# Kernel optimization log

Measured on AMD Instinct MI355X. Metric: run time of the kernel, lower is better.

Reference implementation:

```python
import math
import jax, jax.numpy as jnp
import numpy as np

B, N, D = 8, 2048, 512


def setup_inputs() -> dict:
    key = jax.random.key(0)
    ks = jax.random.split(key, 9)
    s = 1.0 / math.sqrt(D)
    return {
        "x": jax.random.normal(ks[0], (B, N, D), dtype=jnp.float32),
        "adj": jax.random.uniform(ks[1], (B, N, N), dtype=jnp.float32),
        "Wqk": jax.random.normal(ks[2], (D, D), dtype=jnp.float32) * s,
        "bqk": jax.random.normal(ks[3], (D,), dtype=jnp.float32) * s,
        "Wl": jax.random.normal(ks[4], (D, D), dtype=jnp.float32) * s,
        "bl": jax.random.normal(ks[5], (D,), dtype=jnp.float32) * s,
        "Wr": jax.random.normal(ks[6], (D, D), dtype=jnp.float32) * s,
        "Wd": jax.random.normal(ks[7], (D, 1), dtype=jnp.float32),
        "bd": jax.random.normal(ks[8], (D,), dtype=jnp.float32),
    }


def reference(x, adj, Wqk, bqk, Wl, bl, Wr, Wd, bd):
    # degree gating: sigmoid(Linear(rowsum(adj)))
    deg = jnp.sum(adj, axis=-1, keepdims=True)           # [B, N, 1]
    gate = jax.nn.sigmoid(deg * Wd[:, 0] + bd)           # [B, N, D]
    xg = x * gate
    # sigmoid QK features
    QK = jax.nn.sigmoid(xg @ Wqk.T + bqk)                # [B, N, D]
    scores = jnp.einsum("bnd,bmd->bnm", QK, QK) / math.sqrt(D)
    scores = scores * adj                                # adjacency mask
    attn = scores / (jnp.sum(scores, axis=-1, keepdims=True) + 1e-6)
    out = jnp.einsum("bnm,bmd->bnd", attn, xg)           # aggregate values
    out = out @ Wl.T + bl + xg @ Wr.T                    # left + right branch
    return jax.nn.relu(out)
```

## Files before the change

### kernel.cpp

```cpp
#include <hip/hip_runtime.h>
#include <hip/hip_bf16.h>


typedef __bf16 bf16;
typedef __bf16 bf16x8 __attribute__((ext_vector_type(8)));
typedef float  f32x4  __attribute__((ext_vector_type(4)));

#define Bb 8
#define Nn 2048
#define Dd 512
#define SMEM_BYTES 33792

__device__ __forceinline__ bf16 to_bf16(float f) { return (bf16)f; }
__device__ __forceinline__ float sigmoidf_(float x) { return 1.0f / (1.0f + __expf(-x)); }

__device__ __forceinline__ void gld16(const void* g, void* l) {
    __builtin_amdgcn_global_load_lds(
        (__attribute__((address_space(1))) void*)(void*)g,
        (__attribute__((address_space(3))) void*)l,
        16, 0, 0);
}

__device__ __forceinline__ void gemm_bt_core(
    const bf16* __restrict__ A, const bf16* __restrict__ Bt,
    int lda, int ldb, int K,
    char* As, char* Bs, f32x4 acc[4][4])
{
    const int tid  = threadIdx.x;
    const int lane = tid & 63;
    const int wave = tid >> 6;
    const int wm = (wave >> 1) << 6;
    const int wn = (wave & 1) << 6;

    for (int kt = 0; kt < K; kt += 64) {
#pragma unroll
        for (int i = 0; i < 4; ++i) {
            int ff   = i * 256 + tid;
            int row  = ff >> 3;
            int slot = ff & 7;
            int gch  = slot ^ (row & 7);
            gld16(A  + (size_t)row * lda + kt + gch * 8, As + ff * 16);
            gld16(Bt + (size_t)row * ldb + kt + gch * 8, Bs + ff * 16);
        }
        __syncthreads();
#pragma unroll
        for (int ks = 0; ks < 2; ++ks) {
            bf16x8 af[4], bfr[4];
#pragma unroll
            for (int mi = 0; mi < 4; ++mi) {
                int row  = wm + mi * 16 + (lane & 15);
                int slot = ((ks << 2) + (lane >> 4)) ^ (row & 7);
                af[mi] = *(const bf16x8*)(As + row * 128 + slot * 16);
            }
#pragma unroll
            for (int ni = 0; ni < 4; ++ni) {
                int row  = wn + ni * 16 + (lane & 15);
                int slot = ((ks << 2) + (lane >> 4)) ^ (row & 7);
                bfr[ni] = *(const bf16x8*)(Bs + row * 128 + slot * 16);
            }
#pragma unroll
            for (int mi = 0; mi < 4; ++mi)
#pragma unroll
                for (int ni = 0; ni < 4; ++ni)
                    acc[mi][ni] = __builtin_amdgcn_mfma_f32_16x16x32_bf16(
                        af[mi], bfr[ni], acc[mi][ni], 0, 0, 0);
        }
        __syncthreads();
    }
}

#define GEMM_PROLOGUE()                                  \
    __shared__ __align__(16) char smem[SMEM_BYTES];      \
    char* As = smem;                                     \
    char* Bs = smem + 16384;                             \
    f32x4 acc[4][4];                                     \
    _Pragma("unroll") for (int mi = 0; mi < 4; ++mi)     \
    _Pragma("unroll") for (int ni = 0; ni < 4; ++ni)     \
        acc[mi][ni] = (f32x4){0.f, 0.f, 0.f, 0.f};

template <typename F>
__device__ __forceinline__ void epilogue_rt(f32x4 acc[4][4], char* smem, F&& emit)
{
    const int tid  = threadIdx.x;
    const int lane = tid & 63;
    const int wave = tid >> 6;
    const int wm = (wave >> 1) << 6;
    const int wn = (wave & 1) << 6;
    const int cq = lane >> 4;
    const int cl = lane & 15;
    float* t = (float*)smem;
    const int chunk = tid & 15;
    const int rbase = tid >> 4;
#pragma unroll
    for (int ph = 0; ph < 2; ++ph) {
        __syncthreads();
        if ((wm >> 6) == ph) {
#pragma unroll
            for (int mi = 0; mi < 4; ++mi)
#pragma unroll
                for (int ni = 0; ni < 4; ++ni)
#pragma unroll
                    for (int r = 0; r < 4; ++r) {
                        int lr = mi * 16 + cq * 4 + r;
                        int lc = wn + ni * 16 + cl;
                        t[lr * 132 + lc] = acc[mi][ni][r];
                    }
        }
        __syncthreads();
#pragma unroll
        for (int rr = 0; rr < 4; ++rr) {
            int lr = rr * 16 + rbase;
            f32x4 a = *(const f32x4*)&t[lr * 132 + chunk * 8];
            f32x4 b = *(const f32x4*)&t[lr * 132 + chunk * 8 + 4];
            float v[8] = {a[0], a[1], a[2], a[3], b[0], b[1], b[2], b[3]};
            emit(ph * 64 + lr, chunk * 8, v);
        }
    }
}

__global__ __launch_bounds__(256) void k_castw(
    const float* __restrict__ Wqk, const float* __restrict__ Wl,
    const float* __restrict__ Wr,
    bf16* __restrict__ Wqkb, bf16* __restrict__ Wlb, bf16* __restrict__ Wrb)
{
    int i = blockIdx.x * 256 + threadIdx.x;
    Wqkb[i] = to_bf16(Wqk[i]);
    Wlb[i]  = to_bf16(Wl[i]);
    Wrb[i]  = to_bf16(Wr[i]);
}

__global__ __launch_bounds__(256) void k_gate(
    const float* __restrict__ x, const float* __restrict__ adj,
    const float* __restrict__ Wd, const float* __restrict__ bd,
    bf16* __restrict__ xg)
{
    const int rowg = blockIdx.x;
    const float4* arow = (const float4*)(adj + (size_t)rowg * Nn);
    float4 v0 = arow[threadIdx.x];
    float4 v1 = arow[threadIdx.x + 256];
    float s = v0.x + v0.y + v0.z + v0.w + v1.x + v1.y + v1.z + v1.w;
#pragma unroll
    for (int off = 32; off > 0; off >>= 1) s += __shfl_down(s, off, 64);
    __shared__ float red[4];
    if ((threadIdx.x & 63) == 0) red[threadIdx.x >> 6] = s;
    __syncthreads();
    const float deg = red[0] + red[1] + red[2] + red[3];
#pragma unroll
    for (int d = threadIdx.x; d < Dd; d += 256) {
        float g = sigmoidf_(deg * Wd[d] + bd[d]);
        xg[(size_t)rowg * Dd + d] = to_bf16(x[(size_t)rowg * Dd + d] * g);
    }
}

__global__ __launch_bounds__(256) void k_transpose(
    const bf16* __restrict__ xg, bf16* __restrict__ xgT)
{
    const int b = blockIdx.z, nt = blockIdx.y, dt = blockIdx.x;
    __shared__ bf16 tile[64][66];
    const int c = threadIdx.x & 63, r0 = threadIdx.x >> 6;
    const bf16* src = xg + ((size_t)b * Nn + nt * 64) * Dd + dt * 64;
#pragma unroll
    for (int i = 0; i < 16; ++i) {
        int r = i * 4 + r0;
        tile[r][c] = src[(size_t)r * Dd + c];
    }
    __syncthreads();
    bf16* dst = xgT + ((size_t)b * Dd + dt * 64) * Nn + nt * 64;
#pragma unroll
    for (int i = 0; i < 16; ++i) {
        int r = i * 4 + r0;
        dst[(size_t)r * Nn + c] = tile[c][r];
    }
}

__global__ __launch_bounds__(256) void k_qk_gemm(
    const bf16* __restrict__ xg, const bf16* __restrict__ Wqkb,
    const float* __restrict__ bqk, bf16* __restrict__ QK)
{
    const int blockRow = blockIdx.y * 128;
    const int blockCol = blockIdx.x * 128;
    GEMM_PROLOGUE();
    gemm_bt_core(xg + (size_t)blockRow * Dd, Wqkb + (size_t)blockCol * Dd,
                 Dd, Dd, Dd, As, Bs, acc);
    epilogue_rt(acc, smem, [&](int lr, int lc, float* v) {
        int c = blockCol + lc;
        float4 b0 = *(const float4*)(bqk + c);
        float4 b1 = *(const float4*)(bqk + c + 4);
        float bb[8] = {b0.x, b0.y, b0.z, b0.w, b1.x, b1.y, b1.z, b1.w};
        bf16x8 o;
#pragma unroll
        for (int j = 0; j < 8; ++j) o[j] = to_bf16(sigmoidf_(v[j] + bb[j]));
        *(bf16x8*)(QK + (size_t)(blockRow + lr) * Dd + c) = o;
    });
}

__global__ __launch_bounds__(256) void k_s_gemm(
    const bf16* __restrict__ QK, const float* __restrict__ adj,
    bf16* __restrict__ S, float* __restrict__ denom)
{
    const int b = blockIdx.y;
    int t = blockIdx.x, i = 0;
    while (t >= 16 - i) { t -= 16 - i; ++i; }
    const int j = i + t;
    const int rowI = i * 128, rowJ = j * 128;
    const bf16* Qb = QK + (size_t)b * Nn * Dd;
    GEMM_PROLOGUE();
    gemm_bt_core(Qb + (size_t)rowI * Dd, Qb + (size_t)rowJ * Dd,
                 Dd, Dd, Dd, As, Bs, acc);
    const float scale = 0.044194173824159216f;

    const int tid  = threadIdx.x;
    const int lane = tid & 63;
    const int wave = tid >> 6;
    const int wm = (wave >> 1) << 6;
    const int wn = (wave & 1) << 6;
    const int cq = lane >> 4;
    const int cl = lane & 15;
    float* tls = (float*)smem;
    const int chunk = tid & 15;
    const int rbase = tid >> 4;

    auto store_side = [&](int blockRow, int blockCol, bool trans) {
#pragma unroll
        for (int ph = 0; ph < 2; ++ph) {
            __syncthreads();
            if (!trans) {
                if ((wave >> 1) == ph) {
#pragma unroll
                    for (int mi = 0; mi < 4; ++mi)
#pragma unroll
                        for (int ni = 0; ni < 4; ++ni)
#pragma unroll
                            for (int r = 0; r < 4; ++r)
                                tls[(mi * 16 + cq * 4 + r) * 132 + wn + ni * 16 + cl]
                                    = acc[mi][ni][r];
                }
            } else {
                if ((wave & 1) == ph) {
#pragma unroll
                    for (int mi = 0; mi < 4; ++mi)
#pragma unroll
                        for (int ni = 0; ni < 4; ++ni)
#pragma unroll
                            for (int r = 0; r < 4; ++r)
                                tls[(ni * 16 + cl) * 132 + wm + mi * 16 + cq * 4 + r]
                                    = acc[mi][ni][r];
                }
            }
            __syncthreads();
#pragma unroll
            for (int rr = 0; rr < 4; ++rr) {
                int lr = rr * 16 + rbase;
                f32x4 a = *(const f32x4*)&tls[lr * 132 + chunk * 8];
                f32x4 c4 = *(const f32x4*)&tls[lr * 132 + chunk * 8 + 4];
                float v[8] = {a[0], a[1], a[2], a[3], c4[0], c4[1], c4[2], c4[3]};
                int gRow = blockRow + ph * 64 + lr;
                size_t base = ((size_t)b * Nn + gRow) * Nn + blockCol + chunk * 8;
                float4 a0 = *(const float4*)(adj + base);
                float4 a1 = *(const float4*)(adj + base + 4);
                float aa[8] = {a0.x, a0.y, a0.z, a0.w, a1.x, a1.y, a1.z, a1.w};
                bf16x8 o;
                float ds = 0.f;
#pragma unroll
                for (int jj = 0; jj < 8; ++jj) {
                    float s = v[jj] * scale * aa[jj];
                    bf16 sb = to_bf16(s);
                    o[jj] = sb;
                    ds += (float)sb;
                }
                *(bf16x8*)(S + base) = o;
#pragma unroll
                for (int off = 8; off > 0; off >>= 1) ds += __shfl_xor(ds, off, 16);
                if ((tid & 15) == 0) atomicAdd(&denom[b * Nn + gRow], ds);
            }
        }
    };
    store_side(rowI, rowJ, false);
    if (i != j) store_side(rowJ, rowI, true);
}

__global__ __launch_bounds__(256) void k_h_gemm(
    const bf16* __restrict__ S, const bf16* __restrict__ xgT,
    const float* __restrict__ denom, bf16* __restrict__ h)
{
    const int id  = blockIdx.x;
    const int xcd = id & 7;
    const int pos = id >> 3;
    const int xt  = pos & 3;
    const int rg  = xcd * 16 + (pos >> 2);
    const int b   = rg >> 4;
    const int blockRow = (rg & 15) * 128;
    const int blockCol = xt * 128;
    GEMM_PROLOGUE();
    gemm_bt_core(S + ((size_t)b * Nn + blockRow) * Nn,
                 xgT + ((size_t)b * Dd + blockCol) * Nn,
                 Nn, Nn, Nn, As, Bs, acc);
    epilogue_rt(acc, smem, [&](int lr, int lc, float* v) {
        int gRow = blockRow + lr;
        float inv = 1.0f / (denom[b * Nn + gRow] + 1e-6f);
        bf16x8 o;
#pragma unroll
        for (int j = 0; j < 8; ++j) o[j] = to_bf16(v[j] * inv);
        *(bf16x8*)(h + ((size_t)b * Nn + gRow) * Dd + blockCol + lc) = o;
    });
}

__global__ __launch_bounds__(256) void k_out_gemm(
    const bf16* __restrict__ h, const bf16* __restrict__ xg,
    const bf16* __restrict__ Wlb, const bf16* __restrict__ Wrb,
    const float* __restrict__ bl, float* __restrict__ out)
{
    const int blockRow = blockIdx.y * 128;
    const int blockCol = blockIdx.x * 128;
    GEMM_PROLOGUE();
    gemm_bt_core(h  + (size_t)blockRow * Dd, Wlb + (size_t)blockCol * Dd,
                 Dd, Dd, Dd, As, Bs, acc);
    gemm_bt_core(xg + (size_t)blockRow * Dd, Wrb + (size_t)blockCol * Dd,
                 Dd, Dd, Dd, As, Bs, acc);
    epilogue_rt(acc, smem, [&](int lr, int lc, float* v) {
        int c = blockCol + lc;
        float4 b0 = *(const float4*)(bl + c);
        float4 b1 = *(const float4*)(bl + c + 4);
        float bb[8] = {b0.x, b0.y, b0.z, b0.w, b1.x, b1.y, b1.z, b1.w};
        float4 o0, o1;
        o0.x = fmaxf(v[0] + bb[0], 0.f); o0.y = fmaxf(v[1] + bb[1], 0.f);
        o0.z = fmaxf(v[2] + bb[2], 0.f); o0.w = fmaxf(v[3] + bb[3], 0.f);
        o1.x = fmaxf(v[4] + bb[4], 0.f); o1.y = fmaxf(v[5] + bb[5], 0.f);
        o1.z = fmaxf(v[6] + bb[6], 0.f); o1.w = fmaxf(v[7] + bb[7], 0.f);
        float* p = out + (size_t)(blockRow + lr) * Dd + c;
        *(float4*)p = o0;
        *(float4*)(p + 4) = o1;
    });
}

extern "C" void kernel_launch(void* const* d_in, const int* in_sizes, int n_in,
                              void* d_out, int out_size, void* d_ws, size_t ws_size,
                              hipStream_t stream) {
    const float* x   = (const float*)d_in[0];
    const float* adj = (const float*)d_in[1];
    const float* Wqk = (const float*)d_in[2];
    const float* bqk = (const float*)d_in[3];
    const float* Wl  = (const float*)d_in[4];
    const float* bl  = (const float*)d_in[5];
    const float* Wr  = (const float*)d_in[6];
    const float* Wd  = (const float*)d_in[7];
    const float* bd  = (const float*)d_in[8];
    float* out = (float*)d_out;

    char* ws = (char*)d_ws;
    bf16* xg   = (bf16*)ws;  ws += (size_t)Bb * Nn * Dd * 2;
    bf16* xgT  = (bf16*)ws;  ws += (size_t)Bb * Dd * Nn * 2;
    bf16* QK   = (bf16*)ws;  ws += (size_t)Bb * Nn * Dd * 2;
    bf16* S    = (bf16*)ws;  ws += (size_t)Bb * Nn * Nn * 2;
    bf16* Wqkb = (bf16*)ws;  ws += (size_t)Dd * Dd * 2;
    bf16* Wlb  = (bf16*)ws;  ws += (size_t)Dd * Dd * 2;
    bf16* Wrb  = (bf16*)ws;  ws += (size_t)Dd * Dd * 2;
    float* denom = (float*)ws; ws += (size_t)Bb * Nn * 4;
    bf16* h = QK;

    hipMemsetAsync(denom, 0, (size_t)Bb * Nn * sizeof(float), stream);
    k_castw<<<dim3(1024), 256, 0, stream>>>(Wqk, Wl, Wr, Wqkb, Wlb, Wrb);
    k_gate<<<dim3(Bb * Nn), 256, 0, stream>>>(x, adj, Wd, bd, xg);
    k_transpose<<<dim3(Dd / 64, Nn / 64, Bb), 256, 0, stream>>>(xg, xgT);
    k_qk_gemm<<<dim3(Dd / 128, (Bb * Nn) / 128), 256, 0, stream>>>(xg, Wqkb, bqk, QK);
    k_s_gemm<<<dim3(136, Bb), 256, 0, stream>>>(QK, adj, S, denom);
    k_h_gemm<<<dim3(512), 256, 0, stream>>>(S, xgT, denom, h);
    k_out_gemm<<<dim3(Dd / 128, (Bb * Nn) / 128), 256, 0, stream>>>(h, xg, Wlb, Wrb, bl, out);
}
```

Baseline: 389.6 us.

## Use 8-wave 256x128 GEMM tiles with triple-buffered async LDS pipeline

Replaces the 4-wave 128x128 GEMM core used by the QK, aggregation and output GEMMs with an 8-wave 256x128 variant. It uses a triple-buffered global_load_lds pipeline with XOR-swizzled 64-wide K tiles, raised MFMA priority and split barriers, so loads overlap compute and LDS bank conflicts drop. Tile staging and the epilogue are adapted to four row phases, 144KB of dynamic shared memory is enabled once, and the grid is remapped so each batch maps to one XCD. The gate kernel is also vectorised to float2. Larger blocks halve the block count and raise LDS use, which lowers occupancy and may leave CUs underfilled for the smaller GEMMs.

Result: faster. 380.0 us (-2.5%).

```diff
diff --git a/kernel.cpp b/kernel.cpp
--- a/kernel.cpp
+++ b/kernel.cpp
@@ -3,6 +3,7 @@
 
 
 typedef __bf16 bf16;
+typedef __bf16 bf16x2 __attribute__((ext_vector_type(2)));
 typedef __bf16 bf16x8 __attribute__((ext_vector_type(8)));
 typedef float  f32x4  __attribute__((ext_vector_type(4)));
 
@@ -10,6 +11,8 @@
 #define Nn 2048
 #define Dd 512
 #define SMEM_BYTES 33792
+#define TILE8_BYTES 49152
+#define SMEM8_BYTES (3 * TILE8_BYTES)
 
 __device__ __forceinline__ bf16 to_bf16(float f) { return (bf16)f; }
 __device__ __forceinline__ float sigmoidf_(float x) { return 1.0f / (1.0f + __expf(-x)); }
@@ -78,23 +81,100 @@
     _Pragma("unroll") for (int ni = 0; ni < 4; ++ni)     \
         acc[mi][ni] = (f32x4){0.f, 0.f, 0.f, 0.f};
 
-template <typename F>
-__device__ __forceinline__ void epilogue_rt(f32x4 acc[4][4], char* smem, F&& emit)
+__device__ __forceinline__ void gemm_bt8_core(
+    const bf16* __restrict__ A, const bf16* __restrict__ Bt,
+    int lda, int ldb, int K, char* smem, f32x4 acc[4][4])
 {
     const int tid  = threadIdx.x;
     const int lane = tid & 63;
     const int wave = tid >> 6;
     const int wm = (wave >> 1) << 6;
     const int wn = (wave & 1) << 6;
+    const int NT = K >> 6;
+
+    char* bA = smem;
+    char* bB = smem + TILE8_BYTES;
+    char* bC = smem + 2 * TILE8_BYTES;
+
+    auto stage_half = [&](char* base, int t, int half) {
+        const int kt = t << 6;
+#pragma unroll
+        for (int i = 0; i < 2; ++i) {
+            int ff   = (half * 2 + i) * 512 + tid;
+            int row  = ff >> 3;
+            int slot = ff & 7;
+            int gch  = slot ^ (row & 7);
+            gld16(A + (size_t)row * lda + kt + gch * 8, base + ff * 16);
+        }
+        int ff   = half * 512 + tid;
+        int row  = ff >> 3;
+        int slot = ff & 7;
+        int gch  = slot ^ (row & 7);
+        gld16(Bt + (size_t)row * ldb + kt + gch * 8, base + 32768 + ff * 16);
+    };
+
+    stage_half(bA, 0, 0); stage_half(bA, 0, 1);
+    stage_half(bB, 1, 0); stage_half(bB, 1, 1);
+    asm volatile("s_waitcnt vmcnt(6)" ::: "memory");
+    __builtin_amdgcn_s_barrier();
+
+#pragma unroll 1
+    for (int t = 0; t < NT; ++t) {
+#pragma unroll
+        for (int ks = 0; ks < 2; ++ks) {
+            bf16x8 af[4], bfr[4];
+#pragma unroll
+            for (int mi = 0; mi < 4; ++mi) {
+                int row  = wm + mi * 16 + (lane & 15);
+                int slot = ((ks << 2) + (lane >> 4)) ^ (row & 7);
+                af[mi] = *(const bf16x8*)(bA + row * 128 + slot * 16);
+            }
+#pragma unroll
+            for (int ni = 0; ni < 4; ++ni) {
+                int row  = wn + ni * 16 + (lane & 15);
+                int slot = ((ks << 2) + (lane >> 4)) ^ (row & 7);
+                bfr[ni] = *(const bf16x8*)(bA + 32768 + row * 128 + slot * 16);
+            }
+            if (t + 2 < NT) stage_half(bC, t + 2, ks);
+            __builtin_amdgcn_s_barrier();
+            asm volatile("s_waitcnt lgkmcnt(0)" ::: "memory");
+            __builtin_amdgcn_sched_barrier(0);
+            __builtin_amdgcn_s_setprio(1);
+#pragma unroll
+            for (int mi = 0; mi < 4; ++mi)
+#pragma unroll
+                for (int ni = 0; ni < 4; ++ni)
+                    acc[mi][ni] = __builtin_amdgcn_mfma_f32_16x16x32_bf16(
+                        af[mi], bfr[ni], acc[mi][ni], 0, 0, 0);
+            __builtin_amdgcn_s_setprio(0);
+            __builtin_amdgcn_sched_barrier(0);
+            if (ks == 1) {
+                if (t + 2 < NT)      asm volatile("s_waitcnt vmcnt(6)" ::: "memory");
+                else if (t + 1 < NT) asm volatile("s_waitcnt vmcnt(0)" ::: "memory");
+            }
+            __builtin_amdgcn_s_barrier();
+        }
+        char* tmp = bA; bA = bB; bB = bC; bC = tmp;
+    }
+}
+
+template <typename F>
+__device__ __forceinline__ void epilogue_rt8(f32x4 acc[4][4], char* smem, F&& emit)
+{
+    const int tid  = threadIdx.x;
+    const int lane = tid & 63;
+    const int wave = tid >> 6;
+    const int wm4 = wave >> 1;
+    const int wn  = (wave & 1) << 6;
     const int cq = lane >> 4;
     const int cl = lane & 15;
     float* t = (float*)smem;
     const int chunk = tid & 15;
     const int rbase = tid >> 4;
 #pragma unroll
-    for (int ph = 0; ph < 2; ++ph) {
+    for (int ph = 0; ph < 4; ++ph) {
         __syncthreads();
-        if ((wm >> 6) == ph) {
+        if (wm4 == ph) {
 #pragma unroll
             for (int mi = 0; mi < 4; ++mi)
 #pragma unroll
@@ -108,8 +188,8 @@
         }
         __syncthreads();
 #pragma unroll
-        for (int rr = 0; rr < 4; ++rr) {
-            int lr = rr * 16 + rbase;
+        for (int rr = 0; rr < 2; ++rr) {
+            int lr = rr * 32 + rbase;
             f32x4 a = *(const f32x4*)&t[lr * 132 + chunk * 8];
             f32x4 b = *(const f32x4*)&t[lr * 132 + chunk * 8 + 4];
             float v[8] = {a[0], a[1], a[2], a[3], b[0], b[1], b[2], b[3]};
@@ -145,11 +225,14 @@
     if ((threadIdx.x & 63) == 0) red[threadIdx.x >> 6] = s;
     __syncthreads();
     const float deg = red[0] + red[1] + red[2] + red[3];
-#pragma unroll
-    for (int d = threadIdx.x; d < Dd; d += 256) {
-        float g = sigmoidf_(deg * Wd[d] + bd[d]);
-        xg[(size_t)rowg * Dd + d] = to_bf16(x[(size_t)rowg * Dd + d] * g);
-    }
+    const int d2 = threadIdx.x;
+    float2 xv  = ((const float2*)(x + (size_t)rowg * Dd))[d2];
+    float2 wd  = ((const float2*)Wd)[d2];
+    float2 bd2 = ((const float2*)bd)[d2];
+    bf16x2 o;
+    o[0] = to_bf16(xv.x * sigmoidf_(deg * wd.x + bd2.x));
+    o[1] = to_bf16(xv.y * sigmoidf_(deg * wd.y + bd2.y));
+    *(bf16x2*)(xg + (size_t)rowg * Dd + d2 * 2) = o;
 }
 
 __global__ __launch_bounds__(256) void k_transpose(
@@ -173,16 +256,21 @@
     }
 }
 
-__global__ __launch_bounds__(256) void k_qk_gemm(
+__global__ __launch_bounds__(512) void k_qk_gemm8(
     const bf16* __restrict__ xg, const bf16* __restrict__ Wqkb,
     const float* __restrict__ bqk, bf16* __restrict__ QK)
 {
-    const int blockRow = blockIdx.y * 128;
+    extern __shared__ __align__(16) char smem[];
+    const int blockRow = blockIdx.y * 256;
     const int blockCol = blockIdx.x * 128;
-    GEMM_PROLOGUE();
-    gemm_bt_core(xg + (size_t)blockRow * Dd, Wqkb + (size_t)blockCol * Dd,
-                 Dd, Dd, Dd, As, Bs, acc);
-    epilogue_rt(acc, smem, [&](int lr, int lc, float* v) {
+    f32x4 acc[4][4];
+#pragma unroll
+    for (int mi = 0; mi < 4; ++mi)
+#pragma unroll
+        for (int ni = 0; ni < 4; ++ni) acc[mi][ni] = (f32x4){0.f, 0.f, 0.f, 0.f};
+    gemm_bt8_core(xg + (size_t)blockRow * Dd, Wqkb + (size_t)blockCol * Dd,
+                  Dd, Dd, Dd, smem, acc);
+    epilogue_rt8(acc, smem, [&](int lr, int lc, float* v) {
         int c = blockCol + lc;
         float4 b0 = *(const float4*)(bqk + c);
         float4 b1 = *(const float4*)(bqk + c + 4);
@@ -279,23 +367,25 @@
     if (i != j) store_side(rowJ, rowI, true);
 }
 
-__global__ __launch_bounds__(256) void k_h_gemm(
+__global__ __launch_bounds__(512) void k_h_gemm8(
     const bf16* __restrict__ S, const bf16* __restrict__ xgT,
     const float* __restrict__ denom, bf16* __restrict__ h)
 {
+    extern __shared__ __align__(16) char smem[];
     const int id  = blockIdx.x;
-    const int xcd = id & 7;
+    const int b   = id & 7;
     const int pos = id >> 3;
-    const int xt  = pos & 3;
-    const int rg  = xcd * 16 + (pos >> 2);
-    const int b   = rg >> 4;
-    const int blockRow = (rg & 15) * 128;
-    const int blockCol = xt * 128;
-    GEMM_PROLOGUE();
-    gemm_bt_core(S + ((size_t)b * Nn + blockRow) * Nn,
-                 xgT + ((size_t)b * Dd + blockCol) * Nn,
-                 Nn, Nn, Nn, As, Bs, acc);
-    epilogue_rt(acc, smem, [&](int lr, int lc, float* v) {
+    const int blockRow = (pos >> 2) * 256;
+    const int blockCol = (pos & 3) * 128;
+    f32x4 acc[4][4];
+#pragma unroll
+    for (int mi = 0; mi < 4; ++mi)
+#pragma unroll
+        for (int ni = 0; ni < 4; ++ni) acc[mi][ni] = (f32x4){0.f, 0.f, 0.f, 0.f};
+    gemm_bt8_core(S + ((size_t)b * Nn + blockRow) * Nn,
+                  xgT + ((size_t)b * Dd + blockCol) * Nn,
+                  Nn, Nn, Nn, smem, acc);
+    epilogue_rt8(acc, smem, [&](int lr, int lc, float* v) {
         int gRow = blockRow + lr;
         float inv = 1.0f / (denom[b * Nn + gRow] + 1e-6f);
         bf16x8 o;
@@ -305,19 +395,24 @@
     });
 }
 
-__global__ __launch_bounds__(256) void k_out_gemm(
+__global__ __launch_bounds__(512) void k_out_gemm8(
     const bf16* __restrict__ h, const bf16* __restrict__ xg,
     const bf16* __restrict__ Wlb, const bf16* __restrict__ Wrb,
     const float* __restrict__ bl, float* __restrict__ out)
 {
-    const int blockRow = blockIdx.y * 128;
+    extern __shared__ __align__(16) char smem[];
+    const int blockRow = blockIdx.y * 256;
     const int blockCol = blockIdx.x * 128;
-    GEMM_PROLOGUE();
-    gemm_bt_core(h  + (size_t)blockRow * Dd, Wlb + (size_t)blockCol * Dd,
-                 Dd, Dd, Dd, As, Bs, acc);
-    gemm_bt_core(xg + (size_t)blockRow * Dd, Wrb + (size_t)blockCol * Dd,
-                 Dd, Dd, Dd, As, Bs, acc);
-    epilogue_rt(acc, smem, [&](int lr, int lc, float* v) {
+    f32x4 acc[4][4];
+#pragma unroll
+    for (int mi = 0; mi < 4; ++mi)
+#pragma unroll
+        for (int ni = 0; ni < 4; ++ni) acc[mi][ni] = (f32x4){0.f, 0.f, 0.f, 0.f};
+    gemm_bt8_core(h  + (size_t)blockRow * Dd, Wlb + (size_t)blockCol * Dd,
+                  Dd, Dd, Dd, smem, acc);
+    gemm_bt8_core(xg + (size_t)blockRow * Dd, Wrb + (size_t)blockCol * Dd,
+                  Dd, Dd, Dd, smem, acc);
+    epilogue_rt8(acc, smem, [&](int lr, int lc, float* v) {
         int c = blockCol + lc;
         float4 b0 = *(const float4*)(bl + c);
         float4 b1 = *(const float4*)(bl + c + 4);
@@ -358,12 +453,23 @@
     float* denom = (float*)ws; ws += (size_t)Bb * Nn * 4;
     bf16* h = QK;
 
+    static bool attr_done = false;
+    if (!attr_done) {
+        hipFuncSetAttribute((const void*)k_qk_gemm8,
+                            hipFuncAttributeMaxDynamicSharedMemorySize, SMEM8_BYTES);
+        hipFuncSetAttribute((const void*)k_h_gemm8,
+                            hipFuncAttributeMaxDynamicSharedMemorySize, SMEM8_BYTES);
+        hipFuncSetAttribute((const void*)k_out_gemm8,
+                            hipFuncAttributeMaxDynamicSharedMemorySize, SMEM8_BYTES);
+        attr_done = true;
+    }
+
     hipMemsetAsync(denom, 0, (size_t)Bb * Nn * sizeof(float), stream);
     k_castw<<<dim3(1024), 256, 0, stream>>>(Wqk, Wl, Wr, Wqkb, Wlb, Wrb);
     k_gate<<<dim3(Bb * Nn), 256, 0, stream>>>(x, adj, Wd, bd, xg);
     k_transpose<<<dim3(Dd / 64, Nn / 64, Bb), 256, 0, stream>>>(xg, xgT);
-    k_qk_gemm<<<dim3(Dd / 128, (Bb * Nn) / 128), 256, 0, stream>>>(xg, Wqkb, bqk, QK);
+    k_qk_gemm8<<<dim3(Dd / 128, (Bb * Nn) / 256), 512, SMEM8_BYTES, stream>>>(xg, Wqkb, bqk, QK);
     k_s_gemm<<<dim3(136, Bb), 256, 0, stream>>>(QK, adj, S, denom);
-    k_h_gemm<<<dim3(512), 256, 0, stream>>>(S, xgT, denom, h);
-    k_out_gemm<<<dim3(Dd / 128, (Bb * Nn) / 128), 256, 0, stream>>>(h, xg, Wlb, Wrb, bl, out);
-}
+    k_h_gemm8<<<dim3(256), 512, SMEM8_BYTES, stream>>>(S, xgT, denom, h);
+    k_out_gemm8<<<dim3(Dd / 128, (Bb * Nn) / 256), 512, SMEM8_BYTES, stream>>>(h, xg, Wlb, Wrb, bl, out);
+}
```
